# Optimization experiments

Measured on AMD Instinct MI355X. Metric: run time of the kernel, lower is better.

Reference implementation:

```python
import jax, jax.numpy as jnp
import numpy as np

M, K, N = 4096, 4096, 12288
GS = 128                 # quantization group size
G = K // GS              # number of groups
PACK = 8                 # int4 values per int32


def _pack_nibbles(key, shape_packed, axis_len):
    # generate random int4 values and pack 8 per int32 (bit-faithful GPTQ layout)
    nib = jax.random.randint(key, shape_packed[:1] + (PACK,) + shape_packed[1:], 0, 16, dtype=jnp.uint32)
    shifts = (jnp.arange(PACK, dtype=jnp.uint32) * 4)[None, :, None]
    return jnp.sum(nib << shifts, axis=1).astype(jnp.int32)


def setup_inputs() -> dict:
    key = jax.random.key(0)
    k1, k2, k3, k4, k5 = jax.random.split(key, 5)
    x = jax.random.normal(k1, (M, K), dtype=jnp.float32) * 0.05
    qweight = _pack_nibbles(k2, (K // PACK, N), K)          # [K/8, N] int32
    qzeros = _pack_nibbles(k3, (G, N // PACK), N)           # [G, N/8] int32
    scales = jax.random.uniform(k4, (G, N), dtype=jnp.float32, minval=0.001, maxval=0.01)
    bias = jax.random.normal(k5, (N,), dtype=jnp.float32) * 0.01
    return {"x": x, "qweight": qweight, "qzeros": qzeros, "scales": scales, "bias": bias}


def _unpack_rows(q):
    # [R, C] int32 -> [R*8, C] int4 values unpacked along rows
    shifts = (jnp.arange(PACK, dtype=jnp.uint32) * 4)[None, :, None]
    nib = (q.astype(jnp.uint32)[:, None, :] >> shifts) & jnp.uint32(0xF)
    return nib.reshape(q.shape[0] * PACK, q.shape[1])


def _unpack_cols(q):
    # [R, C] int32 -> [R, C*8] int4 values unpacked along columns
    shifts = (jnp.arange(PACK, dtype=jnp.uint32) * 4)[None, None, :]
    nib = (q.astype(jnp.uint32)[:, :, None] >> shifts) & jnp.uint32(0xF)
    return nib.reshape(q.shape[0], q.shape[1] * PACK)


def reference(x, qweight, qzeros, scales, bias):
    # dequantize: w[k,n] = (q[k,n] - (z[g,n]+1)) * s[g,n],  g = k // GS
    q = _unpack_rows(qweight).astype(jnp.float32)                    # [K, N]
    z = (_unpack_cols(qzeros).astype(jnp.float32) + 1.0)             # [G, N]
    s = scales                                                       # [G, N]
    w = (q.reshape(G, GS, N) - z[:, None, :]) * s[:, None, :]        # [G, GS, N]
    w = w.reshape(K, N)
    return x @ w + bias
```

## Files before the change

### kernel.cpp

```cpp
#include <hip/hip_runtime.h>
#include <hip/hip_bf16.h>

namespace {
constexpr int Md = 4096, Kd = 4096, Nd = 12288;
constexpr int BM = 256, BN = 128, BK = 64;
constexpr int TK = Kd / BK;
constexpr int THREADS = 512;
constexpr size_t A_BYTES = (size_t)Md * Kd * 2;
constexpr int LDS_BYTES = (2 * BM * BK + BN * BK) * 2;

typedef __attribute__((ext_vector_type(4))) float f4;
typedef __attribute__((ext_vector_type(8))) short b8;

__device__ __forceinline__ unsigned cvtpk(float lo, float hi) {
  unsigned r;
  asm("v_cvt_pk_bf16_f32 %0, %1, %2" : "=v"(r) : "v"(lo), "v"(hi));
  return r;
}

__global__ __launch_bounds__(256)
void cvtA_kernel(const float* __restrict__ X, unsigned short* __restrict__ Xb, int n8) {
  int i = blockIdx.x * blockDim.x + threadIdx.x;
  const int stride = gridDim.x * blockDim.x;
  for (; i < n8; i += stride) {
    const f4* p = (const f4*)X + (size_t)i * 2;
    f4 a = p[0], b = p[1];
    uint4 o;
    o.x = cvtpk(a[0], a[1]); o.y = cvtpk(a[2], a[3]);
    o.z = cvtpk(b[0], b[1]); o.w = cvtpk(b[2], b[3]);
    ((uint4*)Xb)[i] = o;
  }
}

template<bool AWS>
__global__ __launch_bounds__(THREADS, 4)
void qgemm2(const float* __restrict__ X, const unsigned short* __restrict__ Xb,
            const int* __restrict__ QW, const int* __restrict__ QZ,
            const float* __restrict__ SC, const float* __restrict__ BS,
            float* __restrict__ OUT)
{
  extern __shared__ char smem[];
  unsigned short* As = (unsigned short*)smem;
  unsigned short* Bs = (unsigned short*)(smem + 2 * BM * BK * 2);

  const int nwg = gridDim.x;
  const int cpx = nwg >> 3;
  const int b = blockIdx.x;
  const int swz = (b & 7) * cpx + (b >> 3);
  const int bm = swz / (Nd / BN), bn = swz % (Nd / BN);
  const int m0 = bm * BM, n0 = bn * BN;

  const int tid = threadIdx.x, lane = tid & 63;
  const int wid = tid >> 6;
  const int wr = wid >> 1, wc = wid & 1;

  const int n_l = tid & 127;
  const int k8b = (tid >> 7) * 2;

  f4 acc[4][4];
  #pragma unroll
  for (int i = 0; i < 4; ++i)
    #pragma unroll
    for (int j = 0; j < 4; ++j) acc[i][j] = {0.0f, 0.0f, 0.0f, 0.0f};

  auto stageA = [&](int t, int buf) {
    #pragma unroll
    for (int i = 0; i < 4; ++i) {
      const int c = i * THREADS + tid;
      const int r = c >> 3, kbl = c & 7;
      const unsigned short* src = Xb + (size_t)(m0 + r) * Kd + t * BK + ((kbl ^ (r & 7)) << 3);
      __builtin_amdgcn_global_load_lds(
          (const __attribute__((address_space(1))) unsigned*)src,
          (__attribute__((address_space(3))) unsigned*)(As + buf * BM * BK + c * 8),
          16, 0, 0);
    }
  };
  auto stageA_f = [&](int t, int buf) {
    #pragma unroll
    for (int i = 0; i < 4; ++i) {
      const int c = i * THREADS + tid;
      const int r = c >> 3, kbl = c & 7;
      const f4* src = (const f4*)(X + (size_t)(m0 + r) * Kd + t * BK + ((kbl ^ (r & 7)) << 3));
      f4 a = src[0], bb = src[1];
      uint4 o;
      o.x = cvtpk(a[0], a[1]); o.y = cvtpk(a[2], a[3]);
      o.z = cvtpk(bb[0], bb[1]); o.w = cvtpk(bb[2], bb[3]);
      *(uint4*)(As + buf * BM * BK + c * 8) = o;
    }
  };

  auto loadB = [&](int t, int* w, float& s, float& negc) {
    const int* qp = QW + (size_t)(t * 8 + k8b) * Nd + n0 + n_l;
    w[0] = qp[0];
    w[1] = qp[Nd];
    const int g = t >> 1;
    s = SC[(size_t)g * Nd + n0 + n_l];
    const int nab = n0 + n_l;
    const int z32 = QZ[(size_t)g * (Nd / 8) + (nab >> 3)];
    const int z = (z32 >> ((nab & 7) * 4)) & 15;
    negc = -(float)(z + 1) * s;
  };
  auto writeB = [&](const int* w, float s, float negc) {
    #pragma unroll
    for (int i = 0; i < 2; ++i) {
      const unsigned q = (unsigned)w[i];
      const int k8 = k8b + i;
      float f[8];
      #pragma unroll
      for (int j = 0; j < 8; ++j)
        f[j] = __builtin_fmaf((float)((q >> (4 * j)) & 15u), s, negc);
      uint4 o;
      o.x = cvtpk(f[0], f[1]); o.y = cvtpk(f[2], f[3]);
      o.z = cvtpk(f[4], f[5]); o.w = cvtpk(f[6], f[7]);
      const int chunk = (k8 ^ (n_l & 7)) << 3;
      *(uint4*)(Bs + n_l * BK + chunk) = o;
    }
  };

  int bw[2]; float sS, sNC;
  int nbw[2]; float nS, nNC;

  if constexpr (AWS) stageA(0, 0); else stageA_f(0, 0);
  loadB(0, bw, sS, sNC);
  writeB(bw, sS, sNC);
  __syncthreads();

  for (int t = 0; t < TK; ++t) {
    const int cb = t & 1;
    if (t + 1 < TK) {
      if constexpr (AWS) stageA(t + 1, cb ^ 1);
      loadB(t + 1, nbw, nS, nNC);
    }
    #pragma unroll
    for (int ks = 0; ks < 2; ++ks) {
      b8 af[4], bf[4];
      const int kb = ks * 4 + (lane >> 4);
      #pragma unroll
      for (int mi = 0; mi < 4; ++mi) {
        const int r = wr * 64 + mi * 16 + (lane & 15);
        af[mi] = *(const b8*)&As[cb * BM * BK + r * BK + ((kb ^ (r & 7)) << 3)];
      }
      #pragma unroll
      for (int ni = 0; ni < 4; ++ni) {
        const int cc = wc * 64 + ni * 16 + (lane & 15);
        bf[ni] = *(const b8*)&Bs[cc * BK + ((kb ^ (cc & 7)) << 3)];
      }
      #pragma unroll
      for (int mi = 0; mi < 4; ++mi)
        #pragma unroll
        for (int ni = 0; ni < 4; ++ni)
          acc[mi][ni] = __builtin_amdgcn_mfma_f32_16x16x32_bf16(af[mi], bf[ni], acc[mi][ni], 0, 0, 0);
    }
    __syncthreads();
    if (t + 1 < TK) {
      if constexpr (!AWS) stageA_f(t + 1, cb ^ 1);
      writeB(nbw, nS, nNC);
    }
    __syncthreads();
  }

  #pragma unroll
  for (int ni = 0; ni < 4; ++ni) {
    const int gn = n0 + wc * 64 + ni * 16 + (lane & 15);
    const float bv = BS[gn];
    #pragma unroll
    for (int mi = 0; mi < 4; ++mi) {
      const int gm = m0 + wr * 64 + mi * 16 + ((lane >> 4) << 2);
      #pragma unroll
      for (int j = 0; j < 4; ++j)
        OUT[(size_t)(gm + j) * Nd + gn] = acc[mi][ni][j] + bv;
    }
  }
}
}

extern "C" void kernel_launch(void* const* d_in, const int* in_sizes, int n_in,
                              void* d_out, int out_size, void* d_ws, size_t ws_size,
                              hipStream_t stream) {
  const float* x  = (const float*)d_in[0];
  const int*   qw = (const int*)d_in[1];
  const int*   qz = (const int*)d_in[2];
  const float* sc = (const float*)d_in[3];
  const float* bs = (const float*)d_in[4];
  float* out = (float*)d_out;

  (void)hipFuncSetAttribute((const void*)qgemm2<true>,
                            hipFuncAttributeMaxDynamicSharedMemorySize, LDS_BYTES);
  (void)hipFuncSetAttribute((const void*)qgemm2<false>,
                            hipFuncAttributeMaxDynamicSharedMemorySize, LDS_BYTES);

  dim3 grid((Md / BM) * (Nd / BN));
  if (ws_size >= A_BYTES) {
    unsigned short* xb = (unsigned short*)d_ws;
    const int n8 = Md * Kd / 8;
    cvtA_kernel<<<2048, 256, 0, stream>>>(x, xb, n8);
    qgemm2<true><<<grid, dim3(THREADS), LDS_BYTES, stream>>>(x, xb, qw, qz, sc, bs, out);
  } else {
    qgemm2<false><<<grid, dim3(THREADS), LDS_BYTES, stream>>>(x, nullptr, qw, qz, sc, bs, out);
  }
}
```

Baseline: 411.2 us.

## Double-buffer dequantized B tiles and unroll K loop by two

Gives B its own double buffer in LDS so the dequantized weight tile for the next step is written before the current MFMA work instead of after a barrier. The K loop is unrolled by two so each scale/zero load serves one 128-wide group. The qweight load for the step after next is issued early. This aims to overlap B dequantization with MFMA compute, at the cost of more LDS and a launch bound lowered from 4 to 2 blocks, which may reduce occupancy.

New measurement: 589.8 us. 1.43x slower.

```diff
diff --git a/kernel.cpp b/kernel.cpp
--- a/kernel.cpp
+++ b/kernel.cpp
@@ -7,7 +7,9 @@
 constexpr int TK = Kd / BK;
 constexpr int THREADS = 512;
 constexpr size_t A_BYTES = (size_t)Md * Kd * 2;
-constexpr int LDS_BYTES = (2 * BM * BK + BN * BK) * 2;
+constexpr int AS_T = BM * BK;
+constexpr int BS_T = BN * BK;
+constexpr int LDS_BYTES = (2 * AS_T + 2 * BS_T) * 2;
 
 typedef __attribute__((ext_vector_type(4))) float f4;
 typedef __attribute__((ext_vector_type(8))) short b8;
@@ -33,15 +35,15 @@
 }
 
 template<bool AWS>
-__global__ __launch_bounds__(THREADS, 4)
-void qgemm2(const float* __restrict__ X, const unsigned short* __restrict__ Xb,
+__global__ __launch_bounds__(THREADS, 2)
+void qgemm3(const float* __restrict__ X, const unsigned short* __restrict__ Xb,
             const int* __restrict__ QW, const int* __restrict__ QZ,
             const float* __restrict__ SC, const float* __restrict__ BS,
             float* __restrict__ OUT)
 {
   extern __shared__ char smem[];
   unsigned short* As = (unsigned short*)smem;
-  unsigned short* Bs = (unsigned short*)(smem + 2 * BM * BK * 2);
+  unsigned short* Bs = (unsigned short*)(smem + 2 * AS_T * 2);
 
   const int nwg = gridDim.x;
   const int cpx = nwg >> 3;
@@ -71,7 +73,7 @@
       const unsigned short* src = Xb + (size_t)(m0 + r) * Kd + t * BK + ((kbl ^ (r & 7)) << 3);
       __builtin_amdgcn_global_load_lds(
           (const __attribute__((address_space(1))) unsigned*)src,
-          (__attribute__((address_space(3))) unsigned*)(As + buf * BM * BK + c * 8),
+          (__attribute__((address_space(3))) unsigned*)(As + buf * AS_T + c * 8),
           16, 0, 0);
     }
   };
@@ -85,22 +87,23 @@
       uint4 o;
       o.x = cvtpk(a[0], a[1]); o.y = cvtpk(a[2], a[3]);
       o.z = cvtpk(bb[0], bb[1]); o.w = cvtpk(bb[2], bb[3]);
-      *(uint4*)(As + buf * BM * BK + c * 8) = o;
-    }
-  };
-
-  auto loadB = [&](int t, int* w, float& s, float& negc) {
+      *(uint4*)(As + buf * AS_T + c * 8) = o;
+    }
+  };
+
+  auto loadQW = [&](int t, int* w) {
     const int* qp = QW + (size_t)(t * 8 + k8b) * Nd + n0 + n_l;
     w[0] = qp[0];
     w[1] = qp[Nd];
-    const int g = t >> 1;
+  };
+  auto loadSZ = [&](int g, float& s, float& negc) {
     s = SC[(size_t)g * Nd + n0 + n_l];
     const int nab = n0 + n_l;
     const int z32 = QZ[(size_t)g * (Nd / 8) + (nab >> 3)];
     const int z = (z32 >> ((nab & 7) * 4)) & 15;
     negc = -(float)(z + 1) * s;
   };
-  auto writeB = [&](const int* w, float s, float negc) {
+  auto writeB = [&](const int* w, float s, float negc, int buf) {
     #pragma unroll
     for (int i = 0; i < 2; ++i) {
       const unsigned q = (unsigned)w[i];
@@ -113,24 +116,13 @@
       o.x = cvtpk(f[0], f[1]); o.y = cvtpk(f[2], f[3]);
       o.z = cvtpk(f[4], f[5]); o.w = cvtpk(f[6], f[7]);
       const int chunk = (k8 ^ (n_l & 7)) << 3;
-      *(uint4*)(Bs + n_l * BK + chunk) = o;
-    }
-  };
-
-  int bw[2]; float sS, sNC;
-  int nbw[2]; float nS, nNC;
-
-  if constexpr (AWS) stageA(0, 0); else stageA_f(0, 0);
-  loadB(0, bw, sS, sNC);
-  writeB(bw, sS, sNC);
-  __syncthreads();
-
-  for (int t = 0; t < TK; ++t) {
-    const int cb = t & 1;
-    if (t + 1 < TK) {
-      if constexpr (AWS) stageA(t + 1, cb ^ 1);
-      loadB(t + 1, nbw, nS, nNC);
-    }
+      *(uint4*)(Bs + buf * BS_T + n_l * BK + chunk) = o;
+    }
+  };
+
+  auto mfma_tile = [&](int cb) {
+    const unsigned short* Ab = As + cb * AS_T;
+    const unsigned short* Bb = Bs + cb * BS_T;
     #pragma unroll
     for (int ks = 0; ks < 2; ++ks) {
       b8 af[4], bf[4];
@@ -138,12 +130,12 @@
       #pragma unroll
       for (int mi = 0; mi < 4; ++mi) {
         const int r = wr * 64 + mi * 16 + (lane & 15);
-        af[mi] = *(const b8*)&As[cb * BM * BK + r * BK + ((kb ^ (r & 7)) << 3)];
+        af[mi] = *(const b8*)&Ab[r * BK + ((kb ^ (r & 7)) << 3)];
       }
       #pragma unroll
       for (int ni = 0; ni < 4; ++ni) {
         const int cc = wc * 64 + ni * 16 + (lane & 15);
-        bf[ni] = *(const b8*)&Bs[cc * BK + ((kb ^ (cc & 7)) << 3)];
+        bf[ni] = *(const b8*)&Bb[cc * BK + ((kb ^ (cc & 7)) << 3)];
       }
       #pragma unroll
       for (int mi = 0; mi < 4; ++mi)
@@ -151,12 +143,37 @@
         for (int ni = 0; ni < 4; ++ni)
           acc[mi][ni] = __builtin_amdgcn_mfma_f32_16x16x32_bf16(af[mi], bf[ni], acc[mi][ni], 0, 0, 0);
     }
+  };
+
+  int wE[2], wO[2];
+  float sCur, ncCur, sNxt, ncNxt;
+
+  if constexpr (AWS) stageA(0, 0); else stageA_f(0, 0);
+  loadQW(0, wE);
+  loadSZ(0, sCur, ncCur);
+  writeB(wE, sCur, ncCur, 0);
+  loadQW(1, wO);
+  __syncthreads();
+
+  for (int t = 0; t < TK; t += 2) {
+    if constexpr (AWS) stageA(t + 1, 1); else stageA_f(t + 1, 1);
+    writeB(wO, sCur, ncCur, 1);
+    if (t + 2 < TK) {
+      loadQW(t + 2, wE);
+      loadSZ(t / 2 + 1, sNxt, ncNxt);
+    }
+    mfma_tile(0);
     __syncthreads();
-    if (t + 1 < TK) {
-      if constexpr (!AWS) stageA_f(t + 1, cb ^ 1);
-      writeB(nbw, nS, nNC);
-    }
+
+    if (t + 2 < TK) {
+      if constexpr (AWS) stageA(t + 2, 0); else stageA_f(t + 2, 0);
+      writeB(wE, sNxt, ncNxt, 0);
+    }
+    if (t + 3 < TK) loadQW(t + 3, wO);
+    mfma_tile(1);
     __syncthreads();
+
+    sCur = sNxt; ncCur = ncNxt;
   }
 
   #pragma unroll
@@ -184,9 +201,9 @@
   const float* bs = (const float*)d_in[4];
   float* out = (float*)d_out;
 
-  (void)hipFuncSetAttribute((const void*)qgemm2<true>,
+  (void)hipFuncSetAttribute((const void*)qgemm3<true>,
                             hipFuncAttributeMaxDynamicSharedMemorySize, LDS_BYTES);
-  (void)hipFuncSetAttribute((const void*)qgemm2<false>,
+  (void)hipFuncSetAttribute((const void*)qgemm3<false>,
                             hipFuncAttributeMaxDynamicSharedMemorySize, LDS_BYTES);
 
   dim3 grid((Md / BM) * (Nd / BN));
@@ -194,8 +211,8 @@
     unsigned short* xb = (unsigned short*)d_ws;
     const int n8 = Md * Kd / 8;
     cvtA_kernel<<<2048, 256, 0, stream>>>(x, xb, n8);
-    qgemm2<true><<<grid, dim3(THREADS), LDS_BYTES, stream>>>(x, xb, qw, qz, sc, bs, out);
+    qgemm3<true><<<grid, dim3(THREADS), LDS_BYTES, stream>>>(x, xb, qw, qz, sc, bs, out);
   } else {
-    qgemm2<false><<<grid, dim3(THREADS), LDS_BYTES, stream>>>(x, nullptr, qw, qz, sc, bs, out);
-  }
-}
+    qgemm3<false><<<grid, dim3(THREADS), LDS_BYTES, stream>>>(x, nullptr, qw, qz, sc, bs, out);
+  }
+}
```

## Double-buffer dequantized B tile and use a one-barrier software pipeline

Applied to the files above, without the earlier changes.

The main GEMM kernel now keeps two LDS buffers for the dequantized weight tile as well as for A. The loop is unrolled by two so each step issues the async A load and the next qweight loads, writes the dequantized B for the next tile, runs MFMAs on the current tile, then synchronises with explicit waitcnt plus one s_barrier instead of two __syncthreads. This aims to overlap dequantization and global loads with MFMA work and cut barrier stalls. It raises LDS use and lowers the launch-bounds occupancy hint from 4 to 2, and relies on hand-counted vmcnt values being correct.

Result: slower. 504.3 us (+22.6%).

```diff
diff --git a/kernel.cpp b/kernel.cpp
--- a/kernel.cpp
+++ b/kernel.cpp
@@ -7,10 +7,16 @@
 constexpr int TK = Kd / BK;
 constexpr int THREADS = 512;
 constexpr size_t A_BYTES = (size_t)Md * Kd * 2;
-constexpr int LDS_BYTES = (2 * BM * BK + BN * BK) * 2;
+constexpr int AS_T = BM * BK;
+constexpr int BS_T = BN * BK;
+constexpr int LDS_BYTES = (2 * AS_T + 2 * BS_T) * 2;
+constexpr int LDS_FB    = (2 * AS_T + BS_T) * 2;
 
 typedef __attribute__((ext_vector_type(4))) float f4;
 typedef __attribute__((ext_vector_type(8))) short b8;
+
+#define WAIT_LGKM0 asm volatile("s_waitcnt lgkmcnt(0)" ::: "memory")
+#define WAIT_VM(n) asm volatile("s_waitcnt vmcnt(" #n ")" ::: "memory")
 
 __device__ __forceinline__ unsigned cvtpk(float lo, float hi) {
   unsigned r;
@@ -32,30 +38,26 @@
   }
 }
 
-template<bool AWS>
-__global__ __launch_bounds__(THREADS, 4)
-void qgemm2(const float* __restrict__ X, const unsigned short* __restrict__ Xb,
+__global__ __launch_bounds__(THREADS, 2)
+void qgemm4(const unsigned short* __restrict__ Xb,
             const int* __restrict__ QW, const int* __restrict__ QZ,
             const float* __restrict__ SC, const float* __restrict__ BS,
             float* __restrict__ OUT)
 {
   extern __shared__ char smem[];
   unsigned short* As = (unsigned short*)smem;
-  unsigned short* Bs = (unsigned short*)(smem + 2 * BM * BK * 2);
-
-  const int nwg = gridDim.x;
-  const int cpx = nwg >> 3;
-  const int b = blockIdx.x;
+  unsigned short* Bs = (unsigned short*)(smem + 2 * AS_T * 2);
+
+  const int nwg = gridDim.x, cpx = nwg >> 3, b = blockIdx.x;
   const int swz = (b & 7) * cpx + (b >> 3);
   const int bm = swz / (Nd / BN), bn = swz % (Nd / BN);
   const int m0 = bm * BM, n0 = bn * BN;
 
-  const int tid = threadIdx.x, lane = tid & 63;
-  const int wid = tid >> 6;
+  const int tid = threadIdx.x, lane = tid & 63, wid = tid >> 6;
   const int wr = wid >> 1, wc = wid & 1;
-
   const int n_l = tid & 127;
   const int k8b = (tid >> 7) * 2;
+  const int nab = n0 + n_l;
 
   f4 acc[4][4];
   #pragma unroll
@@ -71,10 +73,153 @@
       const unsigned short* src = Xb + (size_t)(m0 + r) * Kd + t * BK + ((kbl ^ (r & 7)) << 3);
       __builtin_amdgcn_global_load_lds(
           (const __attribute__((address_space(1))) unsigned*)src,
-          (__attribute__((address_space(3))) unsigned*)(As + buf * BM * BK + c * 8),
+          (__attribute__((address_space(3))) unsigned*)(As + buf * AS_T + c * 8),
           16, 0, 0);
     }
   };
+  auto loadQWf = [&](int t, int& w0, int& w1) {
+    const int* qp = QW + (size_t)(t * 8 + k8b) * Nd + nab;
+    w0 = qp[0]; w1 = qp[Nd];
+  };
+  auto loadSZf = [&](int g, float& s, int& z32) {
+    s = SC[(size_t)g * Nd + nab];
+    z32 = QZ[(size_t)g * (Nd / 8) + (nab >> 3)];
+  };
+  auto writeB = [&](int w0, int w1, float s, int z32, int buf) {
+    const int z = (z32 >> ((nab & 7) * 4)) & 15;
+    const float negc = -(float)(z + 1) * s;
+    const int w[2] = {w0, w1};
+    #pragma unroll
+    for (int i = 0; i < 2; ++i) {
+      const unsigned q = (unsigned)w[i];
+      const int k8 = k8b + i;
+      float f[8];
+      #pragma unroll
+      for (int j = 0; j < 8; ++j)
+        f[j] = __builtin_fmaf((float)((q >> (4 * j)) & 15u), s, negc);
+      uint4 o;
+      o.x = cvtpk(f[0], f[1]); o.y = cvtpk(f[2], f[3]);
+      o.z = cvtpk(f[4], f[5]); o.w = cvtpk(f[6], f[7]);
+      *(uint4*)(Bs + buf * BS_T + n_l * BK + ((k8 ^ (n_l & 7)) << 3)) = o;
+    }
+  };
+  auto mfma_tile = [&](int cb) {
+    const unsigned short* Ab = As + cb * AS_T;
+    const unsigned short* Bb = Bs + cb * BS_T;
+    #pragma unroll
+    for (int ks = 0; ks < 2; ++ks) {
+      b8 af[4], bf[4];
+      const int kb = ks * 4 + (lane >> 4);
+      #pragma unroll
+      for (int mi = 0; mi < 4; ++mi) {
+        const int r = wr * 64 + mi * 16 + (lane & 15);
+        af[mi] = *(const b8*)&Ab[r * BK + ((kb ^ (r & 7)) << 3)];
+      }
+      #pragma unroll
+      for (int ni = 0; ni < 4; ++ni) {
+        const int cc = wc * 64 + ni * 16 + (lane & 15);
+        bf[ni] = *(const b8*)&Bb[cc * BK + ((kb ^ (cc & 7)) << 3)];
+      }
+      #pragma unroll
+      for (int mi = 0; mi < 4; ++mi)
+        #pragma unroll
+        for (int ni = 0; ni < 4; ++ni)
+          acc[mi][ni] = __builtin_amdgcn_mfma_f32_16x16x32_bf16(af[mi], bf[ni], acc[mi][ni], 0, 0, 0);
+    }
+  };
+
+  int wE0, wE1, wO0, wO1, zC, zN;
+  float sC, sN;
+
+  loadQWf(0, wE0, wE1);
+  loadSZf(0, sC, zC);
+  stageA(0, 0);
+  writeB(wE0, wE1, sC, zC, 0);
+  loadQWf(1, wO0, wO1);
+  __builtin_amdgcn_sched_barrier(0);
+  WAIT_LGKM0;
+  WAIT_VM(2);
+  __builtin_amdgcn_s_barrier();
+  __builtin_amdgcn_sched_barrier(0);
+
+  for (int t = 0; t + 3 < TK; t += 2) {
+    stageA(t + 1, 1);
+    __builtin_amdgcn_sched_barrier(0);
+    loadQWf(t + 2, wE0, wE1);
+    loadSZf((t >> 1) + 1, sN, zN);
+    writeB(wO0, wO1, sC, zC, 1);
+    mfma_tile(0);
+    __builtin_amdgcn_sched_barrier(0);
+    WAIT_LGKM0;
+    WAIT_VM(4);
+    __builtin_amdgcn_s_barrier();
+    __builtin_amdgcn_sched_barrier(0);
+
+    stageA(t + 2, 0);
+    __builtin_amdgcn_sched_barrier(0);
+    loadQWf(t + 3, wO0, wO1);
+    writeB(wE0, wE1, sN, zN, 0);
+    mfma_tile(1);
+    __builtin_amdgcn_sched_barrier(0);
+    WAIT_LGKM0;
+    WAIT_VM(2);
+    __builtin_amdgcn_s_barrier();
+    __builtin_amdgcn_sched_barrier(0);
+
+    sC = sN; zC = zN;
+  }
+
+  stageA(TK - 1, 1);
+  __builtin_amdgcn_sched_barrier(0);
+  writeB(wO0, wO1, sC, zC, 1);
+  mfma_tile(0);
+  __builtin_amdgcn_sched_barrier(0);
+  WAIT_LGKM0;
+  WAIT_VM(0);
+  __builtin_amdgcn_s_barrier();
+  __builtin_amdgcn_sched_barrier(0);
+  mfma_tile(1);
+
+  #pragma unroll
+  for (int ni = 0; ni < 4; ++ni) {
+    const int gn = n0 + wc * 64 + ni * 16 + (lane & 15);
+    const float bv = BS[gn];
+    #pragma unroll
+    for (int mi = 0; mi < 4; ++mi) {
+      const int gm = m0 + wr * 64 + mi * 16 + ((lane >> 4) << 2);
+      #pragma unroll
+      for (int j = 0; j < 4; ++j)
+        OUT[(size_t)(gm + j) * Nd + gn] = acc[mi][ni][j] + bv;
+    }
+  }
+}
+
+__global__ __launch_bounds__(THREADS, 2)
+void qgemm_fb(const float* __restrict__ X,
+              const int* __restrict__ QW, const int* __restrict__ QZ,
+              const float* __restrict__ SC, const float* __restrict__ BS,
+              float* __restrict__ OUT)
+{
+  extern __shared__ char smem[];
+  unsigned short* As = (unsigned short*)smem;
+  unsigned short* Bs = (unsigned short*)(smem + 2 * AS_T * 2);
+
+  const int nwg = gridDim.x, cpx = nwg >> 3, b = blockIdx.x;
+  const int swz = (b & 7) * cpx + (b >> 3);
+  const int bm = swz / (Nd / BN), bn = swz % (Nd / BN);
+  const int m0 = bm * BM, n0 = bn * BN;
+  const int tid = threadIdx.x, lane = tid & 63, wid = tid >> 6;
+  const int wr = wid >> 1, wc = wid & 1;
+  const int n_l = tid & 127;
+  const int k8b = (tid >> 7) * 2;
+  const int nab = n0 + n_l;
+
+  f4 acc[4][4];
+  #pragma unroll
+  for (int i = 0; i < 4; ++i)
+    #pragma unroll
+    for (int j = 0; j < 4; ++j) acc[i][j] = {0.0f, 0.0f, 0.0f, 0.0f};
+
   auto stageA_f = [&](int t, int buf) {
     #pragma unroll
     for (int i = 0; i < 4; ++i) {
@@ -85,17 +230,14 @@
       uint4 o;
       o.x = cvtpk(a[0], a[1]); o.y = cvtpk(a[2], a[3]);
       o.z = cvtpk(bb[0], bb[1]); o.w = cvtpk(bb[2], bb[3]);
-      *(uint4*)(As + buf * BM * BK + c * 8) = o;
-    }
-  };
-
+      *(uint4*)(As + buf * AS_T + c * 8) = o;
+    }
+  };
   auto loadB = [&](int t, int* w, float& s, float& negc) {
-    const int* qp = QW + (size_t)(t * 8 + k8b) * Nd + n0 + n_l;
-    w[0] = qp[0];
-    w[1] = qp[Nd];
+    const int* qp = QW + (size_t)(t * 8 + k8b) * Nd + nab;
+    w[0] = qp[0]; w[1] = qp[Nd];
     const int g = t >> 1;
-    s = SC[(size_t)g * Nd + n0 + n_l];
-    const int nab = n0 + n_l;
+    s = SC[(size_t)g * Nd + nab];
     const int z32 = QZ[(size_t)g * (Nd / 8) + (nab >> 3)];
     const int z = (z32 >> ((nab & 7) * 4)) & 15;
     negc = -(float)(z + 1) * s;
@@ -112,25 +254,18 @@
       uint4 o;
       o.x = cvtpk(f[0], f[1]); o.y = cvtpk(f[2], f[3]);
       o.z = cvtpk(f[4], f[5]); o.w = cvtpk(f[6], f[7]);
-      const int chunk = (k8 ^ (n_l & 7)) << 3;
-      *(uint4*)(Bs + n_l * BK + chunk) = o;
-    }
-  };
-
-  int bw[2]; float sS, sNC;
-  int nbw[2]; float nS, nNC;
-
-  if constexpr (AWS) stageA(0, 0); else stageA_f(0, 0);
+      *(uint4*)(Bs + n_l * BK + ((k8 ^ (n_l & 7)) << 3)) = o;
+    }
+  };
+
+  int bw[2]; float sS, sNC; int nbw[2]; float nS, nNC;
+  stageA_f(0, 0);
   loadB(0, bw, sS, sNC);
   writeB(bw, sS, sNC);
   __syncthreads();
-
   for (int t = 0; t < TK; ++t) {
     const int cb = t & 1;
-    if (t + 1 < TK) {
-      if constexpr (AWS) stageA(t + 1, cb ^ 1);
-      loadB(t + 1, nbw, nS, nNC);
-    }
+    if (t + 1 < TK) loadB(t + 1, nbw, nS, nNC);
     #pragma unroll
     for (int ks = 0; ks < 2; ++ks) {
       b8 af[4], bf[4];
@@ -138,7 +273,7 @@
       #pragma unroll
       for (int mi = 0; mi < 4; ++mi) {
         const int r = wr * 64 + mi * 16 + (lane & 15);
-        af[mi] = *(const b8*)&As[cb * BM * BK + r * BK + ((kb ^ (r & 7)) << 3)];
+        af[mi] = *(const b8*)&As[cb * AS_T + r * BK + ((kb ^ (r & 7)) << 3)];
       }
       #pragma unroll
       for (int ni = 0; ni < 4; ++ni) {
@@ -153,12 +288,11 @@
     }
     __syncthreads();
     if (t + 1 < TK) {
-      if constexpr (!AWS) stageA_f(t + 1, cb ^ 1);
+      stageA_f(t + 1, cb ^ 1);
       writeB(nbw, nS, nNC);
     }
     __syncthreads();
   }
-
   #pragma unroll
   for (int ni = 0; ni < 4; ++ni) {
     const int gn = n0 + wc * 64 + ni * 16 + (lane & 15);
@@ -184,18 +318,18 @@
   const float* bs = (const float*)d_in[4];
   float* out = (float*)d_out;
 
-  (void)hipFuncSetAttribute((const void*)qgemm2<true>,
+  (void)hipFuncSetAttribute((const void*)qgemm4,
                             hipFuncAttributeMaxDynamicSharedMemorySize, LDS_BYTES);
-  (void)hipFuncSetAttribute((const void*)qgemm2<false>,
-                            hipFuncAttributeMaxDynamicSharedMemorySize, LDS_BYTES);
+  (void)hipFuncSetAttribute((const void*)qgemm_fb,
+                            hipFuncAttributeMaxDynamicSharedMemorySize, LDS_FB);
 
   dim3 grid((Md / BM) * (Nd / BN));
   if (ws_size >= A_BYTES) {
     unsigned short* xb = (unsigned short*)d_ws;
     const int n8 = Md * Kd / 8;
     cvtA_kernel<<<2048, 256, 0, stream>>>(x, xb, n8);
-    qgemm2<true><<<grid, dim3(THREADS), LDS_BYTES, stream>>>(x, xb, qw, qz, sc, bs, out);
+    qgemm4<<<grid, dim3(THREADS), LDS_BYTES, stream>>>(xb, qw, qz, sc, bs, out);
   } else {
-    qgemm2<false><<<grid, dim3(THREADS), LDS_BYTES, stream>>>(x, nullptr, qw, qz, sc, bs, out);
-  }
-}
+    qgemm_fb<<<grid, dim3(THREADS), LDS_FB, stream>>>(x, qw, qz, sc, bs, out);
+  }
+}
```
